# Kernel optimization log

Measured on AMD Instinct MI355X. Metric: run time of the kernel, lower is better.

## Reference

```python
import jax, jax.numpy as jnp
import numpy as np

B, N, ND, H = 8, 1024, 64, 128
NUM_OPS, NUM_PARAMS, SKETCH = 64, 256, 128


def setup_inputs() -> dict:
    key = jax.random.key(0)
    ks = iter(jax.random.split(key, 64))

    def rn(shape, s=0.05):
        return jax.random.normal(next(ks), shape, dtype=jnp.float32) * s

    inp = {
        'node_features': jax.random.normal(next(ks), (B, N, ND), dtype=jnp.float32),
        'adjacency': (jax.random.uniform(next(ks), (B, N, N)) < 0.05).astype(jnp.float32),
        'mask': jnp.ones((B, N), jnp.float32),
    }
    for name, din in (('g1', ND), ('g2', H), ('g3', H)):
        inp[name + '_W'] = rn((din, H))
        inp[name + '_b'] = jnp.zeros((H,), jnp.float32)
        inp[name + '_aW'] = rn((2 * H,))
        inp[name + '_ab'] = jnp.zeros((), jnp.float32)
    for l in (0, 1):
        inp[f'l{l}_Wih'] = rn((4 * H, H))
        inp[f'l{l}_Whh'] = rn((4 * H, H))
        inp[f'l{l}_bih'] = jnp.zeros((4 * H,), jnp.float32)
        inp[f'l{l}_bhh'] = jnp.zeros((4 * H,), jnp.float32)
    for name, dout in (('op', NUM_OPS), ('pa', NUM_PARAMS), ('sk', SKETCH), ('no', ND)):
        inp[name + '_W1'] = rn((H, H))
        inp[name + '_b1'] = jnp.zeros((H,), jnp.float32)
        inp[name + '_W2'] = rn((H, dout))
        inp[name + '_b2'] = jnp.zeros((dout,), jnp.float32)
    return inp


def _gnn(x, adj, W, b, aW, ab):
    # h = Linear(x); att[b,i,j] = sigmoid(aW . [h_j ; h_i] + ab)  (cat order from the torch code)
    h = x @ W + b                      # [B,N,H]
    D = W.shape[1]
    sj = h @ aW[:D]                    # contribution of the dim-1-expanded term (h_j)
    si = h @ aW[D:]                    # contribution of the dim-2-expanded term (h_i)
    att = jax.nn.sigmoid(si[:, :, None] + sj[:, None, :] + ab) * adj  # [B,N,N]
    return jnp.einsum('bij,bjd->bid', att, h)


def _lstm(x, Wih, Whh, bih, bhh):
    # single torch-style LSTM layer, gate order i,f,g,o; zero initial state
    Bx, Hh = x.shape[0], Whh.shape[1]

    def step(carry, xt):
        h, c = carry
        g = xt @ Wih.T + h @ Whh.T + (bih + bhh)       # [B,4H]
        i, f, gg, o = jnp.split(g, 4, axis=-1)
        c = jax.nn.sigmoid(f) * c + jax.nn.sigmoid(i) * jnp.tanh(gg)
        h = jax.nn.sigmoid(o) * jnp.tanh(c)
        return (h, c), h

    z = jnp.zeros((Bx, Hh), x.dtype)
    _, ys = jax.lax.scan(step, (z, z), jnp.swapaxes(x, 0, 1))
    return jnp.swapaxes(ys, 0, 1)


def _mlp(x, W1, b1, W2, b2):
    return jax.nn.relu(x @ W1 + b1) @ W2 + b2


def reference(node_features, adjacency, mask,
              g1_W, g1_b, g1_aW, g1_ab,
              g2_W, g2_b, g2_aW, g2_ab,
              g3_W, g3_b, g3_aW, g3_ab,
              l0_Wih, l0_Whh, l0_bih, l0_bhh,
              l1_Wih, l1_Whh, l1_bih, l1_bhh,
              op_W1, op_b1, op_W2, op_b2,
              pa_W1, pa_b1, pa_W2, pa_b2,
              sk_W1, sk_b1, sk_W2, sk_b2,
              no_W1, no_b1, no_W2, no_b2):
    h = jax.nn.relu(_gnn(node_features, adjacency, g1_W, g1_b, g1_aW, g1_ab))
    h = jax.nn.relu(_gnn(h, adjacency, g2_W, g2_b, g2_aW, g2_ab))
    h = _gnn(h, adjacency, g3_W, g3_b, g3_aW, g3_ab)
    lo = _lstm(h, l0_Wih, l0_Whh, l0_bih, l0_bhh)
    lo = _lstm(lo, l1_Wih, l1_Whh, l1_bih, l1_bhh)
    op_pred = _mlp(lo, op_W1, op_b1, op_W2, op_b2)
    param_pred = _mlp(lo, pa_W1, pa_b1, pa_W2, pa_b2)
    sketch_pred = _mlp(lo, sk_W1, sk_b1, sk_W2, sk_b2)
    node_pred = _mlp(h, no_W1, no_b1, no_W2, no_b2)
    return (op_pred, param_pred, sketch_pred, node_pred)
```

## Files before the change

kernel.cpp:

```cpp
#include <hip/hip_runtime.h>
#include <hip/hip_fp16.h>

typedef __attribute__((ext_vector_type(8))) short short8;
typedef __attribute__((ext_vector_type(4))) float f32x4;
typedef __attribute__((ext_vector_type(2))) unsigned int u32x2;

__device__ __forceinline__ unsigned short bf16_of(float f) {
    unsigned u = __builtin_bit_cast(unsigned, f);
    u += 0x7fffu + ((u >> 16) & 1u);
    return (unsigned short)(u >> 16);
}
__device__ __forceinline__ unsigned bf16pk(float a, float b) {
    return (unsigned)bf16_of(a) | ((unsigned)bf16_of(b) << 16);
}
__device__ __forceinline__ unsigned fp16pk(float a, float b) {
    return __builtin_bit_cast(unsigned, __builtin_amdgcn_cvt_pkrtz(a, b));
}
__device__ __forceinline__ f32x4 h4f(u32x2 v) {
    __half2 a = __builtin_bit_cast(__half2, v[0]);
    __half2 b = __builtin_bit_cast(__half2, v[1]);
    float2 fa = __half22float2(a), fb = __half22float2(b);
    f32x4 r; r[0] = fa.x; r[1] = fa.y; r[2] = fb.x; r[3] = fb.y;
    return r;
}
__device__ __forceinline__ float fexp2(float x) { return __builtin_amdgcn_exp2f(x); }
__device__ __forceinline__ float frcp(float x) { return __builtin_amdgcn_rcpf(x); }
__device__ __forceinline__ float sigm(float x) { return frcp(1.f + fexp2(-1.44269504f * x)); }
__device__ __forceinline__ f32x4 mfma16(short8 a, short8 b, f32x4 c) {
    return __builtin_amdgcn_mfma_f32_16x16x32_bf16(a, b, c, 0, 0, 0);
}
__device__ __forceinline__ float dpp_shr8(float x) {
    return __builtin_bit_cast(float, __builtin_amdgcn_update_dpp(
        0, __builtin_bit_cast(int, x), 0x118, 0xF, 0xF, true));
}
__device__ __forceinline__ float dpp_shl8(float x) {
    return __builtin_bit_cast(float, __builtin_amdgcn_update_dpp(
        0, __builtin_bit_cast(int, x), 0x108, 0xF, 0xF, true));
}

struct PrepArgs {
    const float* src[8];
    unsigned short* dst[8];
    int N[8];
};

__global__ __launch_bounds__(256) void gemm_gnn(
    const float* __restrict__ A, const float* __restrict__ B,
    const float* __restrict__ bias, const float* __restrict__ aW,
    unsigned short* __restrict__ hT, float* __restrict__ siP,
    float* __restrict__ sjP, int K,
    PrepArgs pa, const float* __restrict__ wih,
    unsigned short* __restrict__ wihB, int* __restrict__ flags)
{
    const int tid = threadIdx.x;
    if (blockIdx.y >= 256) {
        const int pid = (blockIdx.y - 256) * 2 + blockIdx.x;
        if (pid < 8) {
            const float* src = pa.src[pid];
            unsigned short* dst = pa.dst[pid];
            const int N = pa.N[pid];
            const int n0 = tid >> 4, kc = (tid & 15) * 8;
            for (int n = n0; n < N; n += 16) {
                unsigned o[4];
#pragma unroll
                for (int e = 0; e < 8; e += 2)
                    o[e >> 1] = bf16pk(src[(size_t)(kc + e) * N + n],
                                       src[(size_t)(kc + e + 1) * N + n]);
                *(u32x2*)&dst[n * 128 + kc] = *(u32x2*)&o[0];
                *(u32x2*)&dst[n * 128 + kc + 4] = *(u32x2*)&o[2];
            }
        } else if (pid == 8) {
            if (tid < 19) flags[tid] = 0;
        } else if (pid < 13) {
            const int base = (pid - 9) * 16384;
            for (int i = tid * 8; i < 16384; i += 2048) {
                const float* s = wih + base + i;
                f32x4 v0 = *(const f32x4*)s, v1 = *(const f32x4*)(s + 4);
                short8 o;
#pragma unroll
                for (int j = 0; j < 4; ++j) {
                    o[j] = (short)bf16_of(v0[j]);
                    o[4 + j] = (short)bf16_of(v1[j]);
                }
                *(short8*)(wihB + base + i) = o;
            }
        }
        return;
    }

    __shared__ float As[32][33];
    __shared__ float Bs[32][68];
    __shared__ unsigned short T[32][70];
    const int tx = tid & 15, ty = tid >> 4;
    const int m0 = blockIdx.y * 32, n0 = blockIdx.x * 64;
    float acc[2][4];
#pragma unroll
    for (int i = 0; i < 2; ++i)
#pragma unroll
        for (int j = 0; j < 4; ++j) acc[i][j] = 0.f;

    for (int k0 = 0; k0 < K; k0 += 32) {
        __syncthreads();
        {
            const int r = tid >> 3, kk = (tid & 7) * 4;
            f32x4 v = *(const f32x4*)(A + (size_t)(m0 + r) * K + k0 + kk);
#pragma unroll
            for (int e = 0; e < 4; ++e) As[r][kk + e] = v[e];
        }
        {
            const int kk = tid >> 3, nn = (tid & 7) * 8;
            const float* src = B + (size_t)(k0 + kk) * 128 + n0 + nn;
            f32x4 v0 = *(const f32x4*)src;
            f32x4 v1 = *(const f32x4*)(src + 4);
#pragma unroll
            for (int e = 0; e < 4; ++e) { Bs[kk][nn + e] = v0[e]; Bs[kk][nn + 4 + e] = v1[e]; }
        }
        __syncthreads();
#pragma unroll 8
        for (int k = 0; k < 32; ++k) {
            float a0 = As[ty * 2 + 0][k], a1 = As[ty * 2 + 1][k];
            f32x4 bv = *(const f32x4*)&Bs[k][tx * 4];
#pragma unroll
            for (int j = 0; j < 4; ++j) {
                acc[0][j] += a0 * bv[j];
                acc[1][j] += a1 * bv[j];
            }
        }
    }
    f32x4 bv = *(const f32x4*)&bias[n0 + tx * 4];
#pragma unroll
    for (int i = 0; i < 2; ++i)
#pragma unroll
        for (int j = 0; j < 4; ++j) acc[i][j] += bv[j];

    f32x4 wj = *(const f32x4*)&aW[n0 + tx * 4];
    f32x4 wi = *(const f32x4*)&aW[128 + n0 + tx * 4];
#pragma unroll
    for (int i = 0; i < 2; ++i) {
        float pj = acc[i][0] * wj[0] + acc[i][1] * wj[1] + acc[i][2] * wj[2] + acc[i][3] * wj[3];
        float pi = acc[i][0] * wi[0] + acc[i][1] * wi[1] + acc[i][2] * wi[2] + acc[i][3] * wi[3];
#pragma unroll
        for (int o = 8; o > 0; o >>= 1) {
            pj += __shfl_xor(pj, o);
            pi += __shfl_xor(pi, o);
        }
        if (tx == 0) {
            const int m = m0 + ty * 2 + i;
            sjP[blockIdx.x * 8192 + m] = pj;
            siP[blockIdx.x * 8192 + m] = pi;
        }
    }

#pragma unroll
    for (int i = 0; i < 2; ++i) {
        unsigned* tp = (unsigned*)&T[ty * 2 + i][tx * 4];
        tp[0] = bf16pk(acc[i][0], acc[i][1]);
        tp[1] = bf16pk(acc[i][2], acc[i][3]);
    }
    __syncthreads();
    const int b = m0 >> 10, node0 = m0 & 1023;
    const int dr = tid >> 4, npair = tid & 15;
#pragma unroll
    for (int rr = 0; rr < 4; ++rr) {
        const int d = rr * 16 + dr;
        unsigned o = (unsigned)T[npair * 2][d] | ((unsigned)T[npair * 2 + 1][d] << 16);
        *(unsigned*)(hT + ((size_t)b * 128 + n0 + d) * 1024 + node0 + npair * 2) = o;
    }
}

__global__ __launch_bounds__(256) void gnn_agg(
    const float* __restrict__ adj, const unsigned short* __restrict__ hT,
    const float* __restrict__ siP, const float* __restrict__ sjP,
    const float* __restrict__ abp, float* __restrict__ out, int RELU)
{
    __shared__ __align__(16) unsigned short Alds[32 * 40];
    __shared__ __align__(16) unsigned short Blds[128 * 40];
    __shared__ float sjL[1024];
    const int b = blockIdx.y, it = blockIdx.x;
    const int i0 = it * 32;
    const int tid = threadIdx.x, lane = tid & 63, w = tid >> 6;
    const int quad = lane >> 4, col = lane & 15;
    const int rh = w & 1, nh = w >> 1;
    const float ab = abp[0];
    const float* adjb = adj + (size_t)b * 1024 * 1024;
    const unsigned short* hTb = hT + (size_t)b * 128 * 1024;

    for (int j = tid; j < 1024; j += 256)
        sjL[j] = sjP[b * 1024 + j] + sjP[8192 + b * 1024 + j];

    const int ar_ = tid >> 3, ash = (tid & 7) * 4;
    const int br_ = tid >> 1, bsh = (tid & 1) * 16;
    const float sii = siP[b * 1024 + i0 + ar_] + siP[8192 + b * 1024 + i0 + ar_] + ab;

    const float* aptr = adjb + (size_t)(i0 + ar_) * 1024 + ash;
    const unsigned short* bptr = hTb + (size_t)br_ * 1024 + bsh;

    f32x4 paA = *(const f32x4*)(aptr);
    short8 pbA0 = *(const short8*)(bptr);
    short8 pbA1 = *(const short8*)(bptr + 8);
    f32x4 paB = *(const f32x4*)(aptr + 32);
    short8 pbB0 = *(const short8*)(bptr + 32);
    short8 pbB1 = *(const short8*)(bptr + 40);

    f32x4 acc[4] = {};

    for (int j0 = 0; j0 < 1024; j0 += 64) {
        __syncthreads();
        {
            float s0 = sigm(sii + sjL[j0 + ash + 0]) * paA[0];
            float s1 = sigm(sii + sjL[j0 + ash + 1]) * paA[1];
            float s2 = sigm(sii + sjL[j0 + ash + 2]) * paA[2];
            float s3 = sigm(sii + sjL[j0 + ash + 3]) * paA[3];
            u32x2 o = {bf16pk(s0, s1), bf16pk(s2, s3)};
            *(u32x2*)&Alds[ar_ * 40 + ash] = o;
            *(short8*)&Blds[br_ * 40 + bsh] = pbA0;
            *(short8*)&Blds[br_ * 40 + bsh + 8] = pbA1;
        }
        if (j0 + 64 < 1024) {
            paA = *(const f32x4*)(aptr + j0 + 64);
            pbA0 = *(const short8*)(bptr + j0 + 64);
            pbA1 = *(const short8*)(bptr + j0 + 72);
        }
        __syncthreads();
        {
            short8 af = *(const short8*)&Alds[(rh * 16 + col) * 40 + quad * 8];
#pragma unroll
            for (int nt = 0; nt < 4; ++nt) {
                short8 bf = *(const short8*)&Blds[((nh * 4 + nt) * 16 + col) * 40 + quad * 8];
                acc[nt] = mfma16(af, bf, acc[nt]);
            }
        }
        __syncthreads();
        {
            float s0 = sigm(sii + sjL[j0 + 32 + ash + 0]) * paB[0];
            float s1 = sigm(sii + sjL[j0 + 32 + ash + 1]) * paB[1];
            float s2 = sigm(sii + sjL[j0 + 32 + ash + 2]) * paB[2];
            float s3 = sigm(sii + sjL[j0 + 32 + ash + 3]) * paB[3];
            u32x2 o = {bf16pk(s0, s1), bf16pk(s2, s3)};
            *(u32x2*)&Alds[ar_ * 40 + ash] = o;
            *(short8*)&Blds[br_ * 40 + bsh] = pbB0;
            *(short8*)&Blds[br_ * 40 + bsh + 8] = pbB1;
        }
        if (j0 + 96 < 1024) {
            paB = *(const f32x4*)(aptr + j0 + 96);
            pbB0 = *(const short8*)(bptr + j0 + 96);
            pbB1 = *(const short8*)(bptr + j0 + 104);
        }
        __syncthreads();
        {
            short8 af = *(const short8*)&Alds[(rh * 16 + col) * 40 + quad * 8];
#pragma unroll
            for (int nt = 0; nt < 4; ++nt) {
                short8 bf = *(const short8*)&Blds[((nh * 4 + nt) * 16 + col) * 40 + quad * 8];
                acc[nt] = mfma16(af, bf, acc[nt]);
            }
        }
    }
    const int ibase = i0 + rh * 16 + quad * 4;
#pragma unroll
    for (int nt = 0; nt < 4; ++nt) {
        const int d = (nh * 4 + nt) * 16 + col;
#pragma unroll
        for (int r = 0; r < 4; ++r) {
            float v = acc[nt][r];
            if (RELU) v = fmaxf(v, 0.f);
            out[((size_t)b * 1024 + ibase + r) * 128 + d] = v;
        }
    }
}


struct HeadArgs {
    const unsigned short* W1T[4];
    const float* b1[4];
    const unsigned short* W2T[4];
    const float* b2[4];
    float* outp[4];
};

__device__ __forceinline__ void lstm_epilogue(
    const f32x4 accs[4], f32x4 xv0, f32x4 xv1, float* cst, float* hv,
    bool lo, float selLo)
{
    float t0[4], t1[4];
#pragma unroll
    for (int i = 0; i < 4; ++i) {
        float P0 = (lo ? accs[0][i] : dpp_shr8(accs[1][i])) + xv0[i];
        float P1 = (lo ? accs[2][i] : dpp_shr8(accs[3][i])) + xv1[i];
        P1 = fmaxf(P1, -30.f);
        t0[i] = frcp(1.f + fexp2(-1.44269504f * P0));
        float u = fexp2(-2.88539008f * P1);
        t1[i] = (1.f - selLo * u) * frcp(1.f + u);
    }
    float c2[4], og[4];
#pragma unroll
    for (int i = 0; i < 4; ++i) {
        float ig = t0[i];
        float fg = dpp_shl8(t0[i]);
        float gg = t1[i];
        og[i] = dpp_shl8(t1[i]);
        c2[i] = fg * cst[i] + ig * gg;
        cst[i] = c2[i];
    }
    float pc0 = lo ? c2[0] : dpp_shr8(c2[1]);
    float pc1 = lo ? c2[2] : dpp_shr8(c2[3]);
    pc0 = fmaxf(pc0, -30.f);
    pc1 = fmaxf(pc1, -30.f);
    float u0 = fexp2(-2.88539008f * pc0);
    float tc0 = (1.f - u0) * frcp(1.f + u0);
    float u1 = fexp2(-2.88539008f * pc1);
    float tc1 = (1.f - u1) * frcp(1.f + u1);
    float th[4] = {tc0, dpp_shl8(tc0), tc1, dpp_shl8(tc1)};
#pragma unroll
    for (int i = 0; i < 4; ++i) hv[i] = og[i] * th[i];
}

template <int SINK>
__device__ __forceinline__ void lstm_step(
    unsigned short* Hc, unsigned short* Hn, const short8 afr[4][4],
    f32x4 xv0, f32x4 xv1, float* cst, unsigned short* __restrict__ sink,
    int t, int col, int quad, int h4, int b)
{
    short8 bfr[4];
#pragma unroll
    for (int c = 0; c < 4; ++c)
        bfr[c] = *(const short8*)&Hc[col * 136 + c * 32 + quad * 8];
    f32x4 accs[4] = {};
#pragma unroll
    for (int c = 0; c < 4; ++c)
#pragma unroll
        for (int g = 0; g < 4; ++g)
            accs[g] = mfma16(afr[g][c], bfr[c], accs[g]);

    const bool lo = (col < 8);
    const float selLo = lo ? 1.f : 0.f;
    float hv[4];
    lstm_epilogue(accs, xv0, xv1, cst, hv, lo, selLo);
    if (lo) {
        u32x2 hb = {bf16pk(hv[0], hv[1]), bf16pk(hv[2], hv[3])};
        *(u32x2*)&Hn[b * 136 + h4] = hb;
        if (SINK == 0)
            *(u32x2*)(sink + (size_t)t * 1024 + b * 128 + h4) = hb;
        else
            *(u32x2*)(sink + ((size_t)t * 8 + b) * 128 + h4) = hb;
    }
    __builtin_amdgcn_s_waitcnt(0xC07F);
    __builtin_amdgcn_s_barrier();
}

template <int A32, int LROWS>
__device__ void head_strip(
    const void* __restrict__ Asrc, int row0,
    const unsigned short* __restrict__ W1T, const float* __restrict__ b1,
    const unsigned short* __restrict__ W2T, const float* __restrict__ b2,
    float* __restrict__ outp, int dout, unsigned short* A2, int tid)
{
    const int lane = tid & 63, w = tid >> 6;
    const int quad = lane >> 4, col = lane & 15;
    const int mrow = w * 16 + col;
    f32x4 acc[8] = {};
#pragma unroll
    for (int kc = 0; kc < 4; ++kc) {
        short8 af;
        if (A32) {
            const float* s = (const float*)Asrc + (size_t)(row0 + mrow) * 128 + kc * 32 + quad * 8;
            f32x4 v0 = *(const f32x4*)s, v1 = *(const f32x4*)(s + 4);
            short8 v;
#pragma unroll
            for (int j = 0; j < 4; ++j) {
                v[j] = (short)bf16_of(v0[j]);
                v[4 + j] = (short)bf16_of(v1[j]);
            }
            af = v;
        } else {
            af = *(const short8*)((const unsigned short*)Asrc +
                                  (size_t)(row0 + mrow) * 128 + kc * 32 + quad * 8);
        }
#pragma unroll
        for (int nt = 0; nt < 8; ++nt) {
            short8 bf = *(const short8*)&W1T[(nt * 16 + col) * 128 + kc * 32 + quad * 8];
            acc[nt] = mfma16(af, bf, acc[nt]);
        }
    }
    float b1v[8];
#pragma unroll
    for (int nt = 0; nt < 8; ++nt) b1v[nt] = b1[nt * 16 + col];
    __syncthreads();
#pragma unroll
    for (int nt = 0; nt < 8; ++nt)
#pragma unroll
        for (int i = 0; i < 4; ++i) {
            const int mm = w * 16 + quad * 4 + i;
            A2[mm * 136 + nt * 16 + col] = bf16_of(fmaxf(acc[nt][i] + b1v[nt], 0.f));
        }
    __syncthreads();
    const int ntiles = dout >> 4;
    for (int np = 0; np < ntiles; np += 8) {
        const int nts = (ntiles - np < 8) ? ntiles - np : 8;
        f32x4 acc2[8] = {};
#pragma unroll
        for (int kc = 0; kc < 4; ++kc) {
            short8 a2f = *(const short8*)&A2[mrow * 136 + kc * 32 + quad * 8];
            for (int nt = 0; nt < nts; ++nt) {
                short8 bf = *(const short8*)&W2T[((np + nt) * 16 + col) * 128 + kc * 32 + quad * 8];
                acc2[nt] = mfma16(a2f, bf, acc2[nt]);
            }
        }
        for (int nt = 0; nt < nts; ++nt) {
            const int n = (np + nt) * 16 + col;
            const float bb = b2[n];
#pragma unroll
            for (int i = 0; i < 4; ++i) {
                const int r = row0 + w * 16 + quad * 4 + i;
                size_t off;
                if (LROWS) off = ((size_t)(r & 7) * 1024 + (r >> 3)) * dout + n;
                else       off = (size_t)r * dout + n;
                outp[off] = acc2[nt][i] + bb;
            }
        }
    }
}

__global__ __launch_bounds__(512, 2) void lstm_pipe(
    const __half* __restrict__ xw0, const float* __restrict__ Whh0,
    const float* __restrict__ Wih1, const float* __restrict__ Whh1,
    const float* __restrict__ bih1, const float* __restrict__ bhh1,
    unsigned short* __restrict__ hbuf, __half* __restrict__ xw1,
    int* __restrict__ flags, unsigned short* __restrict__ out1b,
    const float* __restrict__ bufH3, HeadArgs ha,
    const float* __restrict__ bih0, const float* __restrict__ bhh0,
    const unsigned short* __restrict__ WihB)
{
    __shared__ __align__(16) unsigned short H[2][16 * 136];
    __shared__ __align__(16) unsigned short A2[128 * 136];
    const int tid = threadIdx.x;
    const int lane = tid & 63;
    const int w = tid >> 6;
    const int quad = lane >> 4;
    const int col = lane & 15;
    const int b = col & 7;
    const int prA = col >> 3;
    const int h4 = w * 16 + quad * 4;

    if (blockIdx.x >= 11) {
        const int wid = blockIdx.x - 11;
        unsigned short* hA = A2;
        const float gsc = (w >= 6) ? 0.5f : 1.f;
        float bs[4];
#pragma unroll
        for (int nt = 0; nt < 4; ++nt) {
            const int n = w * 64 + nt * 16 + col;
            bs[nt] = bih0[n] + bhh0[n];
        }
        for (int idx = wid; idx < 128; idx += 16) {
            const int g = idx >> 3, bq = idx & 7;
            const int row0 = bq * 1024 + g * 64;
            {
                const int r = tid >> 3, c0 = (tid & 7) * 16;
                const float* src = bufH3 + (size_t)(row0 + r) * 128 + c0;
                unsigned short* dst = hA + r * 136 + c0;
#pragma unroll
                for (int e = 0; e < 16; e += 8) {
                    f32x4 v0 = *(const f32x4*)(src + e);
                    f32x4 v1 = *(const f32x4*)(src + e + 4);
                    short8 o;
#pragma unroll
                    for (int j = 0; j < 4; ++j) {
                        o[j] = (short)bf16_of(v0[j]);
                        o[4 + j] = (short)bf16_of(v1[j]);
                    }
                    *(short8*)(dst + e) = o;
                }
            }
            __syncthreads();
#pragma unroll
            for (int rt = 0; rt < 4; ++rt) {
                short8 af[4];
#pragma unroll
                for (int c = 0; c < 4; ++c)
                    af[c] = *(const short8*)&hA[(rt * 16 + col) * 136 + c * 32 + quad * 8];
                f32x4 acc[4] = {};
#pragma unroll
                for (int c = 0; c < 4; ++c)
#pragma unroll
                    for (int nt = 0; nt < 4; ++nt) {
                        short8 bf = *(const short8*)&WihB[(size_t)(w * 64 + nt * 16 + col) * 128 + c * 32 + quad * 8];
                        acc[nt] = mfma16(af[c], bf, acc[nt]);
                    }
#pragma unroll
                for (int nt = 0; nt < 4; ++nt) {
                    const int pr = w >> 1;
                    const int h = (w & 1) * 64 + nt * 16 + col;
#pragma unroll
                    for (int i = 0; i < 4; ++i) {
                        const int t_ = g * 64 + rt * 16 + quad * 4 + i;
                        __half* dst = (__half*)xw0 +
                            (((size_t)t_ * 4 + pr) * 8 + bq) * 128 + h;
                        *dst = (__half)((acc[nt][i] + bs[nt]) * gsc);
                    }
                }
            }
            __builtin_amdgcn_s_waitcnt(0x0F70);
            __builtin_amdgcn_s_barrier();
            if (tid == 0)
                __hip_atomic_fetch_add(&flags[3 + g], 1, __ATOMIC_RELEASE,
                                       __HIP_MEMORY_SCOPE_AGENT);
        }
        return;
    }

    if (blockIdx.x >= 3) {
        const int wid = blockIdx.x - 3;
        for (int s = wid; s < 64; s += 8)
            head_strip<1, 0>(bufH3, s * 128, ha.W1T[3], ha.b1[3],
                             ha.W2T[3], ha.b2[3], ha.outp[3], 64, A2, tid);
        for (int s = wid; s < 64; s += 8) {
            if (tid == 0) {
                while (__hip_atomic_load(&flags[2], __ATOMIC_ACQUIRE,
                                         __HIP_MEMORY_SCOPE_AGENT) < s + 1)
                    __builtin_amdgcn_s_sleep(16);
            }
            __syncthreads();
            head_strip<0, 1>(out1b, s * 128, ha.W1T[0], ha.b1[0],
                             ha.W2T[0], ha.b2[0], ha.outp[0], 64, A2, tid);
            head_strip<0, 1>(out1b, s * 128, ha.W1T[1], ha.b1[1],
                             ha.W2T[1], ha.b2[1], ha.outp[1], 256, A2, tid);
            head_strip<0, 1>(out1b, s * 128, ha.W1T[2], ha.b1[2],
                             ha.W2T[2], ha.b2[2], ha.outp[2], 128, A2, tid);
        }
        return;
    }

    if (blockIdx.x == 1) {
        short8 afrI[4][4];
        f32x4 biasv[4];
#pragma unroll
        for (int g = 0; g < 4; ++g) {
            const float gsc = (g == 3) ? 0.5f : 1.f;
            const int row = g * 128 + w * 16 + col;
#pragma unroll
            for (int c = 0; c < 4; ++c) {
                const float* src = Wih1 + row * 128 + c * 32 + quad * 8;
                short8 v;
#pragma unroll
                for (int j = 0; j < 8; ++j) v[j] = (short)bf16_of(src[j] * gsc);
                afrI[g][c] = v;
            }
            const int rb = g * 128 + w * 16 + quad * 4;
            f32x4 b1 = *(const f32x4*)&bih1[rb];
            f32x4 b2 = *(const f32x4*)&bhh1[rb];
#pragma unroll
            for (int e = 0; e < 4; ++e) biasv[g][e] = (b1[e] + b2[e]) * gsc;
        }
        for (int k = 0; k < 64; ++k) {
            if (tid == 0) {
                while (__hip_atomic_load(&flags[0], __ATOMIC_ACQUIRE,
                                         __HIP_MEMORY_SCOPE_AGENT) < k + 1)
                    __builtin_amdgcn_s_sleep(2);
                if (k >= 4) {
                    while (__hip_atomic_load(&flags[2], __ATOMIC_RELAXED,
                                             __HIP_MEMORY_SCOPE_AGENT) < k - 3)
                        __builtin_amdgcn_s_sleep(2);
                }
            }
            __builtin_amdgcn_s_waitcnt(0xC07F);
            __builtin_amdgcn_s_barrier();
            const unsigned short* hb = hbuf + (size_t)k * 16 * 1024;
            __half* dst = xw1 + (size_t)(k & 3) * 65536;
#pragma unroll 2
            for (int nt = 0; nt < 8; ++nt) {
                const int tl = nt * 2 + (col >> 3);
                const unsigned short* src = hb + tl * 1024 + b * 128 + quad * 8;
                short8 bfr[4];
#pragma unroll
                for (int c = 0; c < 4; ++c) bfr[c] = *(const short8*)&src[c * 32];
                f32x4 acc[4] = {};
#pragma unroll
                for (int c = 0; c < 4; ++c)
#pragma unroll
                    for (int g = 0; g < 4; ++g)
                        acc[g] = mfma16(afrI[g][c], bfr[c], acc[g]);
#pragma unroll
                for (int g = 0; g < 4; ++g) {
                    u32x2 res = {fp16pk(acc[g][0] + biasv[g][0], acc[g][1] + biasv[g][1]),
                                 fp16pk(acc[g][2] + biasv[g][2], acc[g][3] + biasv[g][3])};
                    *(u32x2*)&dst[((tl * 4 + g) * 8 + b) * 128 + w * 16 + quad * 4] = res;
                }
            }
            __builtin_amdgcn_s_waitcnt(0x0F70);
            __builtin_amdgcn_s_barrier();
            if (tid == 0)
                __hip_atomic_store(&flags[1], k + 1, __ATOMIC_RELEASE,
                                   __HIP_MEMORY_SCOPE_AGENT);
        }
        return;
    }

    for (int i = tid; i < 2 * 16 * 136; i += 512) (&H[0][0])[i] = 0;
    float cst[4] = {0.f, 0.f, 0.f, 0.f};
    const int lane_off = (prA * 8 + b) * 128 + h4;

    if (blockIdx.x == 0) {
        short8 afr[4][4];
#pragma unroll
        for (int g = 0; g < 4; ++g) {
            const float gsc = (g == 3) ? 0.5f : 1.f;
            const int row = g * 128 + w * 16 + col;
#pragma unroll
            for (int c = 0; c < 4; ++c) {
                const float* src = Whh0 + row * 128 + c * 32 + quad * 8;
                short8 v;
#pragma unroll
                for (int j = 0; j < 8; ++j) v[j] = (short)bf16_of(src[j] * gsc);
                afr[g][c] = v;
            }
        }
        if (tid == 0) {
            while (__hip_atomic_load(&flags[3], __ATOMIC_ACQUIRE,
                                     __HIP_MEMORY_SCOPE_AGENT) < 8)
                __builtin_amdgcn_s_sleep(2);
        }
        __syncthreads();
        const __half* xp = xw0 + lane_off;
        u32x2 p0a = *(const u32x2*)(xp);
        u32x2 p1a = *(const u32x2*)(xp + 2048);
        u32x2 p0b = *(const u32x2*)(xp + 4096);
        u32x2 p1b = *(const u32x2*)(xp + 6144);
        xp += 8192;
        __syncthreads();

        for (int t = 0; t < 1024; t += 2) {
            if ((t & 63) == 48) {
                const int gw = (t >> 6) + 1;
                if (gw < 16) {
                    if (tid == 0) {
                        while (__hip_atomic_load(&flags[3 + gw], __ATOMIC_ACQUIRE,
                                                 __HIP_MEMORY_SCOPE_AGENT) < 8)
                            __builtin_amdgcn_s_sleep(2);
                    }
                    __builtin_amdgcn_s_waitcnt(0xC07F);
                    __builtin_amdgcn_s_barrier();
                }
            }
            const __half* xr = (t == 1022) ? xp - 8192 : xp;
            {
                f32x4 xv0 = h4f(p0a), xv1 = h4f(p1a);
                p0a = *(const u32x2*)(xr);
                p1a = *(const u32x2*)(xr + 2048);
                lstm_step<0>(&H[0][0], &H[1][0], afr, xv0, xv1, cst, hbuf, t, col, quad, h4, b);
            }
            {
                f32x4 xv0 = h4f(p0b), xv1 = h4f(p1b);
                p0b = *(const u32x2*)(xr + 4096);
                p1b = *(const u32x2*)(xr + 6144);
                lstm_step<0>(&H[1][0], &H[0][0], afr, xv0, xv1, cst, hbuf, t + 1, col, quad, h4, b);
            }
            xp += 8192;
            if ((t & 14) == 14) {
                __syncthreads();
                if (tid == 0)
                    __hip_atomic_store(&flags[0], (t >> 4) + 1, __ATOMIC_RELEASE,
                                       __HIP_MEMORY_SCOPE_AGENT);
            }
        }
    } else {
        short8 afr[4][4];
#pragma unroll
        for (int g = 0; g < 4; ++g) {
            const float gsc = (g == 3) ? 0.5f : 1.f;
            const int row = g * 128 + w * 16 + col;
#pragma unroll
            for (int c = 0; c < 4; ++c) {
                const float* src = Whh1 + row * 128 + c * 32 + quad * 8;
                short8 v;
#pragma unroll
                for (int j = 0; j < 8; ++j) v[j] = (short)bf16_of(src[j] * gsc);
                afr[g][c] = v;
            }
        }
        __syncthreads();
        auto xaddr = [&](int t) -> const __half* {
            return xw1 + (((t >> 4) & 3) * 65536 + (t & 15) * 4096) + lane_off;
        };
        while (__hip_atomic_load(&flags[1], __ATOMIC_ACQUIRE,
                                 __HIP_MEMORY_SCOPE_AGENT) < 2)
            __builtin_amdgcn_s_sleep(2);
        u32x2 p0a = *(const u32x2*)xaddr(0);
        u32x2 p1a = *(const u32x2*)(xaddr(0) + 2048);
        u32x2 p0b = *(const u32x2*)xaddr(1);
        u32x2 p1b = *(const u32x2*)(xaddr(1) + 2048);

        for (int c = 0; c < 64; ++c) {
            if (c > 0) {
                const int target = (c + 2 < 64) ? c + 2 : 64;
                if (tid == 0) {
                    while (__hip_atomic_load(&flags[1], __ATOMIC_ACQUIRE,
                                             __HIP_MEMORY_SCOPE_AGENT) < target)
                        __builtin_amdgcn_s_sleep(2);
                }
                __builtin_amdgcn_s_waitcnt(0xC07F);
                __builtin_amdgcn_s_barrier();
            }
            for (int s = 0; s < 16; s += 2) {
                const int t = c * 16 + s;
                const int t2 = (t + 2 < 1024) ? t + 2 : 1023;
                const int t3 = (t + 3 < 1024) ? t + 3 : 1023;
                {
                    f32x4 xv0 = h4f(p0a), xv1 = h4f(p1a);
                    p0a = *(const u32x2*)xaddr(t2);
                    p1a = *(const u32x2*)(xaddr(t2) + 2048);
                    lstm_step<1>(&H[0][0], &H[1][0], afr, xv0, xv1, cst, out1b, t, col, quad, h4, b);
                }
                {
                    f32x4 xv0 = h4f(p0b), xv1 = h4f(p1b);
                    p0b = *(const u32x2*)xaddr(t3);
                    p1b = *(const u32x2*)(xaddr(t3) + 2048);
                    lstm_step<1>(&H[1][0], &H[0][0], afr, xv0, xv1, cst, out1b, t + 1, col, quad, h4, b);
                }
            }
            __syncthreads();
            if (tid == 0)
                __hip_atomic_store(&flags[2], c + 1, __ATOMIC_RELEASE,
                                   __HIP_MEMORY_SCOPE_AGENT);
        }
    }
}

extern "C" void kernel_launch(void* const* d_in, const int* in_sizes, int n_in,
                              void* d_out, int out_size, void* d_ws, size_t ws_size,
                              hipStream_t stream)
{
    (void)in_sizes; (void)n_in; (void)out_size; (void)ws_size;
    const float* nf    = (const float*)d_in[0];
    const float* adj   = (const float*)d_in[1];
    const float* g1W   = (const float*)d_in[3];
    const float* g1b   = (const float*)d_in[4];
    const float* g1aW  = (const float*)d_in[5];
    const float* g1ab  = (const float*)d_in[6];
    const float* g2W   = (const float*)d_in[7];
    const float* g2b   = (const float*)d_in[8];
    const float* g2aW  = (const float*)d_in[9];
    const float* g2ab  = (const float*)d_in[10];
    const float* g3W   = (const float*)d_in[11];
    const float* g3b   = (const float*)d_in[12];
    const float* g3aW  = (const float*)d_in[13];
    const float* g3ab  = (const float*)d_in[14];
    const float* l0Wih = (const float*)d_in[15];
    const float* l0Whh = (const float*)d_in[16];
    const float* l0bih = (const float*)d_in[17];
    const float* l0bhh = (const float*)d_in[18];
    const float* l1Wih = (const float*)d_in[19];
    const float* l1Whh = (const float*)d_in[20];
    const float* l1bih = (const float*)d_in[21];
    const float* l1bhh = (const float*)d_in[22];
    const float* opW1 = (const float*)d_in[23];
    const float* opb1 = (const float*)d_in[24];
    const float* opW2 = (const float*)d_in[25];
    const float* opb2 = (const float*)d_in[26];
    const float* paW1 = (const float*)d_in[27];
    const float* pab1 = (const float*)d_in[28];
    const float* paW2 = (const float*)d_in[29];
    const float* pab2 = (const float*)d_in[30];
    const float* skW1 = (const float*)d_in[31];
    const float* skb1 = (const float*)d_in[32];
    const float* skW2 = (const float*)d_in[33];
    const float* skb2 = (const float*)d_in[34];
    const float* noW1 = (const float*)d_in[35];
    const float* nob1 = (const float*)d_in[36];
    const float* noW2 = (const float*)d_in[37];
    const float* nob2 = (const float*)d_in[38];

    float* out = (float*)d_out;
    float* ws = (float*)d_ws;
    float* siP   = ws;
    float* sjP   = ws + 16384;
    unsigned short* WihB = (unsigned short*)(ws + 40960);
    float* bufX  = ws + 1048576;
    float* bufH3 = ws + 2097152;
    unsigned short* bufT = (unsigned short*)(ws + 3145728);
    int*  flags = (int*)(ws + 3686400);
    float* xw0f = ws + 3687424;
    float* xw1f = ws + 7881728;
    unsigned short* WT = (unsigned short*)(ws + 8143876);
    unsigned short* out1b = (unsigned short*)(ws + 8209412);
    unsigned short* hbuf = (unsigned short*)bufX;
    __half* xw0 = (__half*)xw0f;
    __half* xw1 = (__half*)xw1f;

    unsigned short* opW1T = WT;
    unsigned short* paW1T = WT + 16384;
    unsigned short* skW1T = WT + 32768;
    unsigned short* noW1T = WT + 49152;
    unsigned short* opW2T = WT + 65536;
    unsigned short* paW2T = WT + 73728;
    unsigned short* skW2T = WT + 106496;
    unsigned short* noW2T = WT + 122880;

    PrepArgs pargs;
    pargs.src[0] = opW1; pargs.dst[0] = opW1T; pargs.N[0] = 128;
    pargs.src[1] = paW1; pargs.dst[1] = paW1T; pargs.N[1] = 128;
    pargs.src[2] = skW1; pargs.dst[2] = skW1T; pargs.N[2] = 128;
    pargs.src[3] = noW1; pargs.dst[3] = noW1T; pargs.N[3] = 128;
    pargs.src[4] = opW2; pargs.dst[4] = opW2T; pargs.N[4] = 64;
    pargs.src[5] = paW2; pargs.dst[5] = paW2T; pargs.N[5] = 256;
    pargs.src[6] = skW2; pargs.dst[6] = skW2T; pargs.N[6] = 128;
    pargs.src[7] = noW2; pargs.dst[7] = noW2T; pargs.N[7] = 64;

    gemm_gnn<<<dim3(2, 263), 256, 0, stream>>>(nf, g1W, g1b, g1aW, bufT, siP, sjP, 64,
                                               pargs, l0Wih, WihB, flags);
    gnn_agg<<<dim3(32, 8), 256, 0, stream>>>(adj, bufT, siP, sjP, g1ab, bufX, 1);
    gemm_gnn<<<dim3(2, 256), 256, 0, stream>>>(bufX, g2W, g2b, g2aW, bufT, siP, sjP, 128,
                                               pargs, l0Wih, WihB, flags);
    gnn_agg<<<dim3(32, 8), 256, 0, stream>>>(adj, bufT, siP, sjP, g2ab, bufX, 1);
    gemm_gnn<<<dim3(2, 256), 256, 0, stream>>>(bufX, g3W, g3b, g3aW, bufT, siP, sjP, 128,
                                               pargs, l0Wih, WihB, flags);
    gnn_agg<<<dim3(32, 8), 256, 0, stream>>>(adj, bufT, siP, sjP, g3ab, bufH3, 0);

    HeadArgs ha;
    ha.W1T[0] = opW1T; ha.b1[0] = opb1; ha.W2T[0] = opW2T; ha.b2[0] = opb2;
    ha.outp[0] = out + 0;
    ha.W1T[1] = paW1T; ha.b1[1] = pab1; ha.W2T[1] = paW2T; ha.b2[1] = pab2;
    ha.outp[1] = out + 524288;
    ha.W1T[2] = skW1T; ha.b1[2] = skb1; ha.W2T[2] = skW2T; ha.b2[2] = skb2;
    ha.outp[2] = out + 2621440;
    ha.W1T[3] = noW1T; ha.b1[3] = nob1; ha.W2T[3] = noW2T; ha.b2[3] = nob2;
    ha.outp[3] = out + 3670016;
    lstm_pipe<<<27, 512, 0, stream>>>(xw0, l0Whh, l1Wih, l1Whh, l1bih, l1bhh,
                                      hbuf, xw1, flags, out1b, bufH3, ha,
                                      l0bih, l0bhh, WihB);
}
```

Measured before the change: 1.310 ms.

## Fuse GNN layers into two persistent kernels with flag-based inter-stage dataflow

Replaces six separate GEMM/aggregation launches with two launches of a fused kernel. Blocks take roles by block index and synchronize through per-batch and per-tile atomic flags, so downstream stages can start as soon as their inputs are ready. Shared memory is unioned across roles, and intermediate buffers are double-buffered to allow overlap. This trades launch gaps and full-grid barriers for spin-wait overhead and a dependence on block scheduling order to avoid deadlock.

```diff
diff --git a/kernel.cpp b/kernel.cpp
--- a/kernel.cpp
+++ b/kernel.cpp
@@ -44,55 +44,35 @@
     int N[8];
 };
 
-__global__ __launch_bounds__(256) void gemm_gnn(
+union SmemF {
+    struct { float As[32][33]; float Bs[32][68]; unsigned short T[32][70]; } g;
+    struct { unsigned short Alds[32 * 40]; unsigned short Blds[128 * 40]; float sjL[1024]; } a;
+};
+
+__device__ __forceinline__ void waitflag(int* p, int target, int tid) {
+    if (tid == 0) {
+        while (__hip_atomic_load(p, __ATOMIC_ACQUIRE, __HIP_MEMORY_SCOPE_AGENT) < target)
+            __builtin_amdgcn_s_sleep(4);
+    }
+    __syncthreads();
+}
+__device__ __forceinline__ void pubflag(int* p, int tid) {
+    __syncthreads();
+    if (tid == 0)
+        __hip_atomic_fetch_add(p, 1, __ATOMIC_RELEASE, __HIP_MEMORY_SCOPE_AGENT);
+}
+
+__device__ void gemm_dev(
     const float* __restrict__ A, const float* __restrict__ B,
     const float* __restrict__ bias, const float* __restrict__ aW,
     unsigned short* __restrict__ hT, float* __restrict__ siP,
-    float* __restrict__ sjP, int K,
-    PrepArgs pa, const float* __restrict__ wih,
-    unsigned short* __restrict__ wihB, int* __restrict__ flags)
+    float* __restrict__ sjP, int K, int bx, int by, int tid, SmemF* sm)
 {
-    const int tid = threadIdx.x;
-    if (blockIdx.y >= 256) {
-        const int pid = (blockIdx.y - 256) * 2 + blockIdx.x;
-        if (pid < 8) {
-            const float* src = pa.src[pid];
-            unsigned short* dst = pa.dst[pid];
-            const int N = pa.N[pid];
-            const int n0 = tid >> 4, kc = (tid & 15) * 8;
-            for (int n = n0; n < N; n += 16) {
-                unsigned o[4];
-#pragma unroll
-                for (int e = 0; e < 8; e += 2)
-                    o[e >> 1] = bf16pk(src[(size_t)(kc + e) * N + n],
-                                       src[(size_t)(kc + e + 1) * N + n]);
-                *(u32x2*)&dst[n * 128 + kc] = *(u32x2*)&o[0];
-                *(u32x2*)&dst[n * 128 + kc + 4] = *(u32x2*)&o[2];
-            }
-        } else if (pid == 8) {
-            if (tid < 19) flags[tid] = 0;
-        } else if (pid < 13) {
-            const int base = (pid - 9) * 16384;
-            for (int i = tid * 8; i < 16384; i += 2048) {
-                const float* s = wih + base + i;
-                f32x4 v0 = *(const f32x4*)s, v1 = *(const f32x4*)(s + 4);
-                short8 o;
-#pragma unroll
-                for (int j = 0; j < 4; ++j) {
-                    o[j] = (short)bf16_of(v0[j]);
-                    o[4 + j] = (short)bf16_of(v1[j]);
-                }
-                *(short8*)(wihB + base + i) = o;
-            }
-        }
-        return;
-    }
-
-    __shared__ float As[32][33];
-    __shared__ float Bs[32][68];
-    __shared__ unsigned short T[32][70];
+    float (*As)[33] = sm->g.As;
+    float (*Bs)[68] = sm->g.Bs;
+    unsigned short (*T)[70] = sm->g.T;
     const int tx = tid & 15, ty = tid >> 4;
-    const int m0 = blockIdx.y * 32, n0 = blockIdx.x * 64;
+    const int m0 = by * 32, n0 = bx * 64;
     float acc[2][4];
 #pragma unroll
     for (int i = 0; i < 2; ++i)
@@ -146,8 +126,8 @@
         }
         if (tx == 0) {
             const int m = m0 + ty * 2 + i;
-            sjP[blockIdx.x * 8192 + m] = pj;
-            siP[blockIdx.x * 8192 + m] = pi;
+            sjP[bx * 8192 + m] = pj;
+            siP[bx * 8192 + m] = pi;
         }
     }
 
@@ -168,17 +148,17 @@
     }
 }
 
-__global__ __launch_bounds__(256) void gnn_agg(
+__device__ void agg_dev(
     const float* __restrict__ adj, const unsigned short* __restrict__ hT,
     const float* __restrict__ siP, const float* __restrict__ sjP,
-    const float* __restrict__ abp, float* __restrict__ out, int RELU)
+    const float* __restrict__ abp, float* __restrict__ out, int RELU,
+    int it, int b, int tid, SmemF* sm)
 {
-    __shared__ __align__(16) unsigned short Alds[32 * 40];
-    __shared__ __align__(16) unsigned short Blds[128 * 40];
-    __shared__ float sjL[1024];
-    const int b = blockIdx.y, it = blockIdx.x;
+    unsigned short* Alds = sm->a.Alds;
+    unsigned short* Blds = sm->a.Blds;
+    float* sjL = sm->a.sjL;
     const int i0 = it * 32;
-    const int tid = threadIdx.x, lane = tid & 63, w = tid >> 6;
+    const int lane = tid & 63, w = tid >> 6;
     const int quad = lane >> 4, col = lane & 15;
     const int rh = w & 1, nh = w >> 1;
     const float ab = abp[0];
@@ -265,6 +245,97 @@
             float v = acc[nt][r];
             if (RELU) v = fmaxf(v, 0.f);
             out[((size_t)b * 1024 + ibase + r) * 128 + d] = v;
+        }
+    }
+}
+
+struct GnnArgs {
+    const float* nf; const float* adj;
+    const float* gW0; const float* gb0; const float* gaW0; const float* gab0;
+    const float* gW1; const float* gb1; const float* gaW1; const float* gab1;
+    const float* gW2; const float* gb2; const float* gaW2; const float* gab2;
+    float* bufX; float* bufH3;
+    unsigned short* hT0; unsigned short* hT1;
+    float* siP0; float* sjP0; float* siP1; float* sjP1;
+    int* gf;
+    const float* wih; unsigned short* wihB;
+    PrepArgs prep;
+};
+
+__global__ __launch_bounds__(256, 5) void gnn_fused(GnnArgs a, int phase)
+{
+    __shared__ __align__(16) SmemF sm;
+    const int bid = blockIdx.x, tid = threadIdx.x;
+    int* fg1 = a.gf;
+    int* fa1 = a.gf + 8;
+    int* fg2 = a.gf + 264;
+    int* fa2 = a.gf + 272;
+    int* fg3 = a.gf + 528;
+
+    if (phase == 0) {
+        if (bid < 512) {
+            const int bx = bid & 1, by = bid >> 1;
+            gemm_dev(a.nf, a.gW0, a.gb0, a.gaW0, a.hT0, a.siP0, a.sjP0, 64,
+                     bx, by, tid, &sm);
+            pubflag(&fg1[by >> 5], tid);
+        } else if (bid < 768) {
+            const int idx = bid - 512, it = idx & 31, b = idx >> 5;
+            waitflag(&fg1[b], 64, tid);
+            agg_dev(a.adj, a.hT0, a.siP0, a.sjP0, a.gab0, a.bufX, 1, it, b, tid, &sm);
+            pubflag(&fa1[idx], tid);
+        } else {
+            const int idx = bid - 768, bx = idx & 1, by = idx >> 1;
+            waitflag(&fa1[by], 1, tid);
+            gemm_dev(a.bufX, a.gW1, a.gb1, a.gaW1, a.hT1, a.siP1, a.sjP1, 128,
+                     bx, by, tid, &sm);
+            pubflag(&fg2[by >> 5], tid);
+        }
+    } else {
+        if (bid < 256) {
+            const int it = bid & 31, b = bid >> 5;
+            waitflag(&fg2[b], 64, tid);
+            agg_dev(a.adj, a.hT1, a.siP1, a.sjP1, a.gab1, a.bufX, 1, it, b, tid, &sm);
+            pubflag(&fa2[bid], tid);
+        } else if (bid < 768) {
+            const int idx = bid - 256, bx = idx & 1, by = idx >> 1;
+            waitflag(&fa2[by], 1, tid);
+            gemm_dev(a.bufX, a.gW2, a.gb2, a.gaW2, a.hT0, a.siP0, a.sjP0, 128,
+                     bx, by, tid, &sm);
+            pubflag(&fg3[by >> 5], tid);
+        } else if (bid < 1024) {
+            const int idx = bid - 768, it = idx & 31, b = idx >> 5;
+            waitflag(&fg3[b], 64, tid);
+            agg_dev(a.adj, a.hT0, a.siP0, a.sjP0, a.gab2, a.bufH3, 0, it, b, tid, &sm);
+        } else {
+            const int pid = bid - 1024;
+            if (pid < 8) {
+                const float* src = a.prep.src[pid];
+                unsigned short* dst = a.prep.dst[pid];
+                const int N = a.prep.N[pid];
+                const int n0 = tid >> 4, kc = (tid & 15) * 8;
+                for (int n = n0; n < N; n += 16) {
+                    unsigned o[4];
+#pragma unroll
+                    for (int e = 0; e < 8; e += 2)
+                        o[e >> 1] = bf16pk(src[(size_t)(kc + e) * N + n],
+                                           src[(size_t)(kc + e + 1) * N + n]);
+                    *(u32x2*)&dst[n * 128 + kc] = *(u32x2*)&o[0];
+                    *(u32x2*)&dst[n * 128 + kc + 4] = *(u32x2*)&o[2];
+                }
+            } else {
+                const int base = (pid - 8) * 16384;
+                for (int i = tid * 8; i < 16384; i += 2048) {
+                    const float* s = a.wih + base + i;
+                    f32x4 v0 = *(const f32x4*)s, v1 = *(const f32x4*)(s + 4);
+                    short8 o;
+#pragma unroll
+                    for (int j = 0; j < 4; ++j) {
+                        o[j] = (short)bf16_of(v0[j]);
+                        o[4 + j] = (short)bf16_of(v1[j]);
+                    }
+                    *(short8*)(a.wihB + base + i) = o;
+                }
+            }
         }
     }
 }
@@ -772,13 +843,15 @@
 
     float* out = (float*)d_out;
     float* ws = (float*)d_ws;
-    float* siP   = ws;
-    float* sjP   = ws + 16384;
-    unsigned short* WihB = (unsigned short*)(ws + 40960);
+    float* siP0  = ws;
+    float* sjP0  = ws + 16384;
+    float* siP1  = ws + 32768;
+    float* sjP1  = ws + 49152;
+    unsigned short* WihB = (unsigned short*)(ws + 65536);
+    int*  gflags = (int*)(ws + 98304);
     float* bufX  = ws + 1048576;
     float* bufH3 = ws + 2097152;
-    unsigned short* bufT = (unsigned short*)(ws + 3145728);
-    int*  flags = (int*)(ws + 3686400);
+    unsigned short* bufT0 = (unsigned short*)(ws + 3145728);
     float* xw0f = ws + 3687424;
     float* xw1f = ws + 7881728;
     unsigned short* WT = (unsigned short*)(ws + 8143876);
@@ -786,6 +859,8 @@
     unsigned short* hbuf = (unsigned short*)bufX;
     __half* xw0 = (__half*)xw0f;
     __half* xw1 = (__half*)xw1f;
+    unsigned short* bufT1 = (unsigned short*)xw0f;
+    int* lflags = gflags + 544;
 
     unsigned short* opW1T = WT;
     unsigned short* paW1T = WT + 16384;
@@ -796,25 +871,29 @@
     unsigned short* skW2T = WT + 106496;
     unsigned short* noW2T = WT + 122880;
 
-    PrepArgs pargs;
-    pargs.src[0] = opW1; pargs.dst[0] = opW1T; pargs.N[0] = 128;
-    pargs.src[1] = paW1; pargs.dst[1] = paW1T; pargs.N[1] = 128;
-    pargs.src[2] = skW1; pargs.dst[2] = skW1T; pargs.N[2] = 128;
-    pargs.src[3] = noW1; pargs.dst[3] = noW1T; pargs.N[3] = 128;
-    pargs.src[4] = opW2; pargs.dst[4] = opW2T; pargs.N[4] = 64;
-    pargs.src[5] = paW2; pargs.dst[5] = paW2T; pargs.N[5] = 256;
-    pargs.src[6] = skW2; pargs.dst[6] = skW2T; pargs.N[6] = 128;
-    pargs.src[7] = noW2; pargs.dst[7] = noW2T; pargs.N[7] = 64;
-
-    gemm_gnn<<<dim3(2, 263), 256, 0, stream>>>(nf, g1W, g1b, g1aW, bufT, siP, sjP, 64,
-                                               pargs, l0Wih, WihB, flags);
-    gnn_agg<<<dim3(32, 8), 256, 0, stream>>>(adj, bufT, siP, sjP, g1ab, bufX, 1);
-    gemm_gnn<<<dim3(2, 256), 256, 0, stream>>>(bufX, g2W, g2b, g2aW, bufT, siP, sjP, 128,
-                                               pargs, l0Wih, WihB, flags);
-    gnn_agg<<<dim3(32, 8), 256, 0, stream>>>(adj, bufT, siP, sjP, g2ab, bufX, 1);
-    gemm_gnn<<<dim3(2, 256), 256, 0, stream>>>(bufX, g3W, g3b, g3aW, bufT, siP, sjP, 128,
-                                               pargs, l0Wih, WihB, flags);
-    gnn_agg<<<dim3(32, 8), 256, 0, stream>>>(adj, bufT, siP, sjP, g3ab, bufH3, 0);
+    GnnArgs ga;
+    ga.nf = nf; ga.adj = adj;
+    ga.gW0 = g1W; ga.gb0 = g1b; ga.gaW0 = g1aW; ga.gab0 = g1ab;
+    ga.gW1 = g2W; ga.gb1 = g2b; ga.gaW1 = g2aW; ga.gab1 = g2ab;
+    ga.gW2 = g3W; ga.gb2 = g3b; ga.gaW2 = g3aW; ga.gab2 = g3ab;
+    ga.bufX = bufX; ga.bufH3 = bufH3;
+    ga.hT0 = bufT0; ga.hT1 = bufT1;
+    ga.siP0 = siP0; ga.sjP0 = sjP0; ga.siP1 = siP1; ga.sjP1 = sjP1;
+    ga.gf = gflags;
+    ga.wih = l0Wih; ga.wihB = WihB;
+    ga.prep.src[0] = opW1; ga.prep.dst[0] = opW1T; ga.prep.N[0] = 128;
+    ga.prep.src[1] = paW1; ga.prep.dst[1] = paW1T; ga.prep.N[1] = 128;
+    ga.prep.src[2] = skW1; ga.prep.dst[2] = skW1T; ga.prep.N[2] = 128;
+    ga.prep.src[3] = noW1; ga.prep.dst[3] = noW1T; ga.prep.N[3] = 128;
+    ga.prep.src[4] = opW2; ga.prep.dst[4] = opW2T; ga.prep.N[4] = 64;
+    ga.prep.src[5] = paW2; ga.prep.dst[5] = paW2T; ga.prep.N[5] = 256;
+    ga.prep.src[6] = skW2; ga.prep.dst[6] = skW2T; ga.prep.N[6] = 128;
+    ga.prep.src[7] = noW2; ga.prep.dst[7] = noW2T; ga.prep.N[7] = 64;
+
+    hipMemsetAsync(gflags, 0, 4096, stream);
+
+    gnn_fused<<<1280, 256, 0, stream>>>(ga, 0);
+    gnn_fused<<<1036, 256, 0, stream>>>(ga, 1);
 
     HeadArgs ha;
     ha.W1T[0] = opW1T; ha.b1[0] = opb1; ha.W2T[0] = opW2T; ha.b2[0] = opb2;
@@ -826,6 +905,6 @@
     ha.W1T[3] = noW1T; ha.b1[3] = nob1; ha.W2T[3] = noW2T; ha.b2[3] = nob2;
     ha.outp[3] = out + 3670016;
     lstm_pipe<<<27, 512, 0, stream>>>(xw0, l0Whh, l1Wih, l1Whh, l1bih, l1bhh,
-                                      hbuf, xw1, flags, out1b, bufH3, ha,
+                                      hbuf, xw1, lflags, out1b, bufH3, ha,
                                       l0bih, l0bhh, WihB);
 }
```

Result: slower. 1.698 ms (+29.6%).
